# Kernel optimization log

Measured on AMD Instinct MI355X. Metric: run time of the kernel, lower is better.

The kernel has to match this reference:

```python
import jax, jax.numpy as jnp
import numpy as np

K_HOPS = 10
ALPHA = 0.1
N_NODES = 50000
N_EDGES = 600000
F_IN = 128
HIDDEN = 64
N_CLASSES = 40


def setup_inputs() -> dict:
    key = jax.random.key(0)
    k1, k2, k3, k4 = jax.random.split(key, 4)
    x = jax.random.normal(k1, (N_NODES, F_IN), dtype=jnp.float32)
    edge_index = jax.random.randint(k2, (2, N_EDGES), 0, N_NODES, dtype=jnp.int32)
    edge_weight = jnp.ones((N_EDGES,), dtype=jnp.float32)
    W1 = jax.random.normal(k3, (F_IN, HIDDEN), dtype=jnp.float32) * (1.0 / np.sqrt(F_IN))
    b1 = jnp.zeros((HIDDEN,), dtype=jnp.float32)
    W2 = jax.random.normal(k4, (HIDDEN, N_CLASSES), dtype=jnp.float32) * (1.0 / np.sqrt(HIDDEN))
    b2 = jnp.zeros((N_CLASSES,), dtype=jnp.float32)
    return {"x": x, "edge_index": edge_index, "edge_weight": edge_weight,
            "W1": W1, "b1": b1, "W2": W2, "b2": b2}


def reference(x, edge_index, edge_weight, W1, b1, W2, b2):
    n = x.shape[0]
    # GCN symmetric normalization with self-loops (tfg gcn cache)
    self_idx = jnp.arange(n, dtype=edge_index.dtype)
    row = jnp.concatenate([edge_index[0], self_idx])
    col = jnp.concatenate([edge_index[1], self_idx])
    w = jnp.concatenate([edge_weight, jnp.ones((n,), dtype=edge_weight.dtype)])
    deg = jax.ops.segment_sum(w, row, num_segments=n)
    dinv = jnp.where(deg > 0, jax.lax.rsqrt(jnp.maximum(deg, 1e-12)), 0.0)
    nw = dinv[row] * w * dinv[col]  # [E+N] normalized edge weights

    def prop(h):
        # h_out[i] = sum_{(i,j)} nw * h[j]
        return jax.ops.segment_sum(h[col] * nw[:, None], row, num_segments=n)

    def step(h, _):
        h_next = prop(h)
        return h_next, None

    # SSGC: out = (1-alpha)/K * sum_{l=1..K} T^l x + alpha * x
    def step_acc(carry, _):
        h, acc = carry
        h_next = prop(h)
        return (h_next, acc + h_next), None

    (_, acc), _ = jax.lax.scan(step_acc, (x, jnp.zeros_like(x)), None, length=K_HOPS)
    h = (1.0 - ALPHA) / K_HOPS * acc + ALPHA * x  # [N, F]

    h = jax.nn.relu(h @ W1 + b1)  # [N, HIDDEN]
    logits = h @ W2 + b2          # [N, N_CLASSES]
    return logits
```

## Files before the change

### kernel.cpp

```cpp
#include <hip/hip_runtime.h>
#include <hip/hip_fp16.h>
#include <math.h>

constexpr int   N   = 50000;
constexpr int   E   = 600000;
constexpr int   FIN = 128;
constexpr int   H   = 64;
constexpr int   C   = 40;
constexpr int   K   = 10;
constexpr float CK  = (1.0f - 0.1f) / 10.0f;
constexpr float AL  = 0.1f;

typedef float v2f __attribute__((ext_vector_type(2)));

__device__ __forceinline__ unsigned pack_fp8x4(float f0, float f1, float f2, float f3) {
    unsigned r = __builtin_amdgcn_cvt_pk_fp8_f32(f0, f1, 0u, false);
    r = __builtin_amdgcn_cvt_pk_fp8_f32(f2, f3, r, true);
    return r;
}

constexpr int G1N  = 64;
constexpr int XPAD = 132;
__global__ __launch_bounds__(256, 2) void k_gemm1(const float* __restrict__ x,
                                                  const float* __restrict__ W1,
                                                  float* __restrict__ y0,
                                                  unsigned char* __restrict__ y0f8) {
    __shared__ float ws[FIN * H];
    __shared__ float xs[G1N * XPAD];
    const float4* W14 = (const float4*)W1;
    const float4* x4  = (const float4*)x;
    int t = threadIdx.x;
    int node0 = blockIdx.x * G1N;
    for (int i = t; i < FIN * H / 4; i += 256) ((float4*)ws)[i] = W14[i];
    for (int p = 0; p < 8; ++p) {
        int idx = p * 256 + t;
        int n   = idx >> 5;
        int kk  = idx & 31;
        int node = node0 + n;
        float4 v = (node < N) ? x4[(size_t)node * (FIN / 4) + kk]
                              : make_float4(0.f, 0.f, 0.f, 0.f);
        *(float4*)(xs + n * XPAD + kk * 4) = v;
    }
    __syncthreads();
    int nb = (t >> 4) * 4;
    int cb = (t & 15) * 4;
    float a00=0,a01=0,a02=0,a03=0, a10=0,a11=0,a12=0,a13=0;
    float a20=0,a21=0,a22=0,a23=0, a30=0,a31=0,a32=0,a33=0;
#pragma unroll 8
    for (int k = 0; k < FIN; ++k) {
        float4 wv = *(const float4*)(ws + k * H + cb);
        float x0 = xs[(nb + 0) * XPAD + k];
        float x1 = xs[(nb + 1) * XPAD + k];
        float x2 = xs[(nb + 2) * XPAD + k];
        float x3 = xs[(nb + 3) * XPAD + k];
        a00 = fmaf(x0, wv.x, a00); a01 = fmaf(x0, wv.y, a01);
        a02 = fmaf(x0, wv.z, a02); a03 = fmaf(x0, wv.w, a03);
        a10 = fmaf(x1, wv.x, a10); a11 = fmaf(x1, wv.y, a11);
        a12 = fmaf(x1, wv.z, a12); a13 = fmaf(x1, wv.w, a13);
        a20 = fmaf(x2, wv.x, a20); a21 = fmaf(x2, wv.y, a21);
        a22 = fmaf(x2, wv.z, a22); a23 = fmaf(x2, wv.w, a23);
        a30 = fmaf(x3, wv.x, a30); a31 = fmaf(x3, wv.y, a31);
        a32 = fmaf(x3, wv.z, a32); a33 = fmaf(x3, wv.w, a33);
    }
    float4 rows[4] = {make_float4(a00,a01,a02,a03), make_float4(a10,a11,a12,a13),
                      make_float4(a20,a21,a22,a23), make_float4(a30,a31,a32,a33)};
#pragma unroll
    for (int i = 0; i < 4; ++i) {
        int node = node0 + nb + i;
        if (node >= N) break;
        float4 r = rows[i];
        *(float4*)(y0 + (size_t)node * H + cb) = r;
        *(unsigned*)(y0f8 + (size_t)node * H + cb) = pack_fp8x4(r.x, r.y, r.z, r.w);
    }
}

__global__ void k_count(const int* __restrict__ row, int* __restrict__ cnt8) {
    int e = blockIdx.x * blockDim.x + threadIdx.x;
    if (e >= E) return;
    atomicAdd(&cnt8[(size_t)(blockIdx.x & 7) * N + row[e]], 1);
}

__global__ __launch_bounds__(1024) void k_scan_blocks(const int* __restrict__ cnt8,
                                                      int* __restrict__ row_ptr,
                                                      int* __restrict__ bsum) {
    __shared__ int s[1024];
    int gid = blockIdx.x * 1024 + threadIdx.x;
    int v = 0;
    if (gid < N) {
#pragma unroll
        for (int c = 0; c < 8; ++c) v += cnt8[(size_t)c * N + gid];
    }
    s[threadIdx.x] = v;
    __syncthreads();
    for (int off = 1; off < 1024; off <<= 1) {
        int t = (threadIdx.x >= off) ? s[threadIdx.x - off] : 0;
        __syncthreads();
        s[threadIdx.x] += t;
        __syncthreads();
    }
    if (gid < N) row_ptr[gid] = s[threadIdx.x] - v;
    if (threadIdx.x == 1023) bsum[blockIdx.x] = s[1023];
}

__global__ void k_scan_sums(const int* __restrict__ bsum, int* __restrict__ boff, int nb) {
    int lane = threadIdx.x;
    int orig = (lane < nb) ? bsum[lane] : 0;
    int v = orig;
    for (int off = 1; off < 64; off <<= 1) {
        int t = __shfl_up(v, off, 64);
        if (lane >= off) v += t;
    }
    if (lane < nb) boff[lane] = v - orig;
}

__global__ __launch_bounds__(1024) void k_addoff(int* __restrict__ row_ptr,
                                                 const int* __restrict__ boff) {
    int gid = blockIdx.x * 1024 + threadIdx.x;
    if (gid < N) row_ptr[gid] += boff[blockIdx.x];
    if (gid == 0) row_ptr[N] = E;
}

__global__ void k_mkoff(const int* __restrict__ row_ptr, int* __restrict__ cnt8) {
    int i = blockIdx.x * blockDim.x + threadIdx.x;
    if (i >= N) return;
    int off = row_ptr[i];
#pragma unroll
    for (int c = 0; c < 8; ++c) {
        int t = cnt8[(size_t)c * N + i];
        cnt8[(size_t)c * N + i] = off;
        off += t;
    }
}

__global__ void k_scatter(const int* __restrict__ row, const int* __restrict__ col,
                          const float* __restrict__ w,
                          int* __restrict__ off8, int2* __restrict__ ep) {
    int e = blockIdx.x * blockDim.x + threadIdx.x;
    if (e >= E) return;
    int r = row[e];
    int p = atomicAdd(&off8[(size_t)(blockIdx.x & 7) * N + r], 1);
    ep[p] = make_int2(col[e], __float_as_int(w[e]));
}

__global__ void k_deg_dinv(const int2* __restrict__ ep, const int* __restrict__ row_ptr,
                           float* __restrict__ dinv, float* __restrict__ dinv2) {
    int i = blockIdx.x * blockDim.x + threadIdx.x;
    if (i >= N) return;
    float d = 1.0f;
    int e0 = row_ptr[i], e1 = row_ptr[i + 1];
    for (int j = e0; j < e1; ++j) d += __int_as_float(ep[j].y);
    float di = rsqrtf(d);
    dinv[i]  = di;
    dinv2[i] = di * di;
}

__global__ __launch_bounds__(256) void k_norm(int2* __restrict__ ep,
                                              const int* __restrict__ row_ptr,
                                              const float* __restrict__ dinv) {
    int node = blockIdx.x * 32 + (threadIdx.x >> 3);
    if (node >= N) return;
    int l = threadIdx.x & 7;
    float dr = dinv[node];
    int e0 = row_ptr[node], e1 = row_ptr[node + 1];
    for (int j = e0 + l; j < e1; j += 8) {
        int2 v = ep[j];
        ep[j] = make_int2(v.x, __float_as_int(__int_as_float(v.y) * dr * dinv[v.x]));
    }
}

constexpr int HSP = 68;
template <bool WRITE_H, bool ACC_INIT, bool FINAL>
__global__ __launch_bounds__(256) void k_prop(const uint2* __restrict__ hin,
                                              uint2* __restrict__ hout,
                                              __half* __restrict__ acch,
                                              const float* __restrict__ dinv2,
                                              const int* __restrict__ row_ptr,
                                              const int2* __restrict__ ep,
                                              const float4* __restrict__ y04,
                                              const float* __restrict__ b1,
                                              const float* __restrict__ W2,
                                              const float* __restrict__ b2,
                                              float* __restrict__ out) {
    extern __shared__ float smem[];
    float* w2s = smem;
    float* hs  = smem + H * C;
    float* b2s = hs + 32 * HSP;
    float* b1s = b2s + C;
    int t = threadIdx.x;
    if (FINAL) {
        for (int i = t; i < H * C; i += 256) w2s[i] = W2[i];
        if (t < C) b2s[t] = b2[t];
        if (t < H) b1s[t] = b1[t];
        __syncthreads();
    }
    int lane = t & 63;
    int nib  = (t >> 6) * 8 + (lane >> 3);
    int l    = lane & 7;
    int node = blockIdx.x * 32 + nib;
    bool nv  = node < N;
    int nodec = nv ? node : N - 1;
    int start = row_ptr[nodec];
    int deg   = nv ? (row_ptr[nodec + 1] - start) : 0;
    int md = deg;
    md = max(md, __shfl_xor(md, 8, 64));
    md = max(md, __shfl_xor(md, 16, 64));
    md = max(md, __shfl_xor(md, 32, 64));
    float s[8];
#pragma unroll
    for (int i = 0; i < 8; ++i) s[i] = 0.0f;
    auto accum = [&](uint2 v, float w) {
        v2f a0 = __builtin_amdgcn_cvt_pk_f32_fp8(v.x, false);
        v2f b0 = __builtin_amdgcn_cvt_pk_f32_fp8(v.x, true);
        v2f a1 = __builtin_amdgcn_cvt_pk_f32_fp8(v.y, false);
        v2f b1v = __builtin_amdgcn_cvt_pk_f32_fp8(v.y, true);
        s[0] = fmaf(w, a0.x, s[0]); s[1] = fmaf(w, a0.y, s[1]);
        s[2] = fmaf(w, b0.x, s[2]); s[3] = fmaf(w, b0.y, s[3]);
        s[4] = fmaf(w, a1.x, s[4]); s[5] = fmaf(w, a1.y, s[5]);
        s[6] = fmaf(w, b1v.x, s[6]); s[7] = fmaf(w, b1v.y, s[7]);
    };
    for (int j = 0; j < md; j += 2) {
        bool a0 = j < deg, a1 = j + 1 < deg;
        int2 e0 = ep[a0 ? start + j     : 0];
        int2 e1 = ep[a1 ? start + j + 1 : 0];
        uint2 v0 = hin[(size_t)e0.x * 8 + l];
        uint2 v1 = hin[(size_t)e1.x * 8 + l];
        float w0 = a0 ? __int_as_float(e0.y) : 0.0f;
        float w1 = a1 ? __int_as_float(e1.y) : 0.0f;
        accum(v0, w0);
        accum(v1, w1);
    }
    if (nv) {
        size_t base = (size_t)node * 8 + l;
        accum(hin[base], dinv2[node]);
        if (WRITE_H) {
            uint2 o;
            o.x = pack_fp8x4(s[0], s[1], s[2], s[3]);
            o.y = pack_fp8x4(s[4], s[5], s[6], s[7]);
            hout[base] = o;
        }
        uint4* ap = (uint4*)(acch + (size_t)node * H + l * 8);
        if (FINAL) {
            uint4 old = *ap;
            const unsigned* u = (const unsigned*)&old;
#pragma unroll
            for (int d = 0; d < 4; ++d) {
                float2 f = __half22float2(*(__half2*)&u[d]);
                s[2*d+0] += f.x; s[2*d+1] += f.y;
            }
            float4 ya = y04[(size_t)node * (H / 4) + 2 * l];
            float4 yb = y04[(size_t)node * (H / 4) + 2 * l + 1];
            const float* bp = b1s + l * 8;
            float* hp = hs + nib * HSP + l * 8;
            hp[0] = fmaxf(fmaf(CK, s[0], fmaf(AL, ya.x, bp[0])), 0.f);
            hp[1] = fmaxf(fmaf(CK, s[1], fmaf(AL, ya.y, bp[1])), 0.f);
            hp[2] = fmaxf(fmaf(CK, s[2], fmaf(AL, ya.z, bp[2])), 0.f);
            hp[3] = fmaxf(fmaf(CK, s[3], fmaf(AL, ya.w, bp[3])), 0.f);
            hp[4] = fmaxf(fmaf(CK, s[4], fmaf(AL, yb.x, bp[4])), 0.f);
            hp[5] = fmaxf(fmaf(CK, s[5], fmaf(AL, yb.y, bp[5])), 0.f);
            hp[6] = fmaxf(fmaf(CK, s[6], fmaf(AL, yb.z, bp[6])), 0.f);
            hp[7] = fmaxf(fmaf(CK, s[7], fmaf(AL, yb.w, bp[7])), 0.f);
        } else {
            if (!ACC_INIT) {
                uint4 old = *ap;
                const unsigned* u = (const unsigned*)&old;
#pragma unroll
                for (int d = 0; d < 4; ++d) {
                    float2 f = __half22float2(*(__half2*)&u[d]);
                    s[2*d+0] += f.x; s[2*d+1] += f.y;
                }
            }
            uint4 nvp;
            unsigned* u = (unsigned*)&nvp;
#pragma unroll
            for (int d = 0; d < 4; ++d) {
                __half2 h = __floats2half2_rn(s[2*d+0], s[2*d+1]);
                u[d] = *(unsigned*)&h;
            }
            *ap = nvp;
        }
    }
    if (FINAL) {
        __syncthreads();
        int node0 = blockIdx.x * 32;
        for (int o = t; o < 32 * C; o += 256) {
            int nl = o / C, c = o % C;
            int n2 = node0 + nl;
            if (n2 >= N) continue;
            float v = b2s[c];
            const float* hr = &hs[nl * HSP];
#pragma unroll
            for (int k = 0; k < H; ++k) v = fmaf(hr[k], w2s[k * C + c], v);
            out[n2 * C + c] = v;
        }
    }
}

extern "C" void kernel_launch(void* const* d_in, const int* in_sizes, int n_in,
                              void* d_out, int out_size, void* d_ws, size_t ws_size,
                              hipStream_t stream) {
    const float* x  = (const float*)d_in[0];
    const int*   ei = (const int*)d_in[1];
    const float* ew = (const float*)d_in[2];
    const float* W1 = (const float*)d_in[3];
    const float* b1 = (const float*)d_in[4];
    const float* W2 = (const float*)d_in[5];
    const float* b2 = (const float*)d_in[6];
    float* out = (float*)d_out;

    const int* row = ei;
    const int* col = ei + E;

    char* ws = (char*)d_ws;
    size_t off = 0;
    auto alloc = [&](size_t bytes) -> char* {
        char* p = ws + off;
        off = (off + bytes + 1023) & ~(size_t)1023;
        return p;
    };
    float*         y0   = (float*)alloc((size_t)N * H * 4);
    unsigned char* y0f8 = (unsigned char*)alloc((size_t)N * H);
    unsigned char* ha   = (unsigned char*)alloc((size_t)N * H);
    unsigned char* hb   = (unsigned char*)alloc((size_t)N * H);
    __half*        acch = (__half*)alloc((size_t)N * H * 2);
    int*   cnt8   = (int*)  alloc((size_t)8 * N * 4);
    float* dinv   = (float*)alloc((size_t)N * 4);
    float* dinv2  = (float*)alloc((size_t)N * 4);
    int*   row_ptr= (int*)  alloc((size_t)(N + 1) * 4);
    int*   bsum   = (int*)  alloc(64 * 4);
    int*   boff   = (int*)  alloc(64 * 4);
    int2*  ep     = (int2*) alloc((size_t)E * 8);

    hipMemsetAsync(cnt8, 0, (size_t)8 * N * 4, stream);

    k_gemm1<<<(N + G1N - 1) / G1N, 256, 0, stream>>>(x, W1, y0, y0f8);

    k_count<<<(E + 255) / 256, 256, 0, stream>>>(row, cnt8);

    constexpr int NB = (N + 1023) / 1024;
    k_scan_blocks<<<NB, 1024, 0, stream>>>(cnt8, row_ptr, bsum);
    k_scan_sums<<<1, 64, 0, stream>>>(bsum, boff, NB);
    k_addoff<<<NB, 1024, 0, stream>>>(row_ptr, boff);
    k_mkoff<<<(N + 255) / 256, 256, 0, stream>>>(row_ptr, cnt8);

    k_scatter<<<(E + 255) / 256, 256, 0, stream>>>(row, col, ew, cnt8, ep);
    k_deg_dinv<<<(N + 255) / 256, 256, 0, stream>>>(ep, row_ptr, dinv, dinv2);
    k_norm<<<(N + 31) / 32, 256, 0, stream>>>(ep, row_ptr, dinv);

    const uint2* hin = (const uint2*)y0f8;
    uint2* bufs[2] = {(uint2*)ha, (uint2*)hb};
    int grid = (N + 31) / 32;
    size_t smemF = (size_t)(H * C + 32 * HSP + C + H) * 4;
    for (int hop = 0; hop < K; ++hop) {
        uint2* hout = bufs[hop & 1];
        if (hop == 0)
            k_prop<true, true, false><<<grid, 256, 0, stream>>>(hin, hout, acch, dinv2,
                row_ptr, ep, (const float4*)y0, b1, W2, b2, out);
        else if (hop == K - 1)
            k_prop<false, false, true><<<grid, 256, smemF, stream>>>(hin, hout, acch, dinv2,
                row_ptr, ep, (const float4*)y0, b1, W2, b2, out);
        else
            k_prop<true, false, false><<<grid, 256, 0, stream>>>(hin, hout, acch, dinv2,
                row_ptr, ep, (const float4*)y0, b1, W2, b2, out);
        hin = hout;
    }
}
```

Measured before the change: 343.4 us.

## Fuse all propagation hops into persistent cooperative kernel with grid sync

Replaces the ten per-hop k_prop launches with a single cooperative kernel, k_hops. It keeps each node's running hop sum in registers across hops and uses grid.sync between hops. This removes the per-hop read and write of the fp16 accumulator buffer, as well as the launch gaps between hops. Each block owns 64 nodes and sorts them by degree so that the 8-lane node groups in a wavefront have similar trip counts. The trade-offs are the cost of nine grid-wide barriers and a requirement that all 782 blocks be co-resident. The occupancy check assumes 256 CUs; if it fails, the code falls back to the old multi-launch path.

```diff
diff --git a/kernel.cpp b/kernel.cpp
--- a/kernel.cpp
+++ b/kernel.cpp
@@ -1,6 +1,9 @@
 #include <hip/hip_runtime.h>
 #include <hip/hip_fp16.h>
+#include <hip/hip_cooperative_groups.h>
 #include <math.h>
+
+namespace cg = cooperative_groups;
 
 constexpr int   N   = 50000;
 constexpr int   E   = 600000;
@@ -168,7 +171,196 @@
     }
 }
 
-constexpr int HSP = 68;
+__device__ __forceinline__ void prop_chunk(const uint2* __restrict__ hin,
+                                           uint2* __restrict__ hout,
+                                           const int2* __restrict__ ep,
+                                           int start, int deg, int md,
+                                           float d2, int nc, bool nv, int l,
+                                           bool writeH, float* acc, float* sout) {
+    float s[8];
+#pragma unroll
+    for (int i = 0; i < 8; ++i) s[i] = 0.f;
+    for (int j = 0; j < md; j += 2) {
+        bool a0 = j < deg, a1 = j + 1 < deg;
+        int2 e0 = ep[a0 ? start + j     : 0];
+        int2 e1 = ep[a1 ? start + j + 1 : 0];
+        uint2 v0 = hin[(size_t)e0.x * 8 + l];
+        uint2 v1 = hin[(size_t)e1.x * 8 + l];
+        float w0 = a0 ? __int_as_float(e0.y) : 0.0f;
+        float w1 = a1 ? __int_as_float(e1.y) : 0.0f;
+        {
+            v2f p0 = __builtin_amdgcn_cvt_pk_f32_fp8(v0.x, false);
+            v2f p1 = __builtin_amdgcn_cvt_pk_f32_fp8(v0.x, true);
+            v2f p2 = __builtin_amdgcn_cvt_pk_f32_fp8(v0.y, false);
+            v2f p3 = __builtin_amdgcn_cvt_pk_f32_fp8(v0.y, true);
+            s[0] = fmaf(w0, p0.x, s[0]); s[1] = fmaf(w0, p0.y, s[1]);
+            s[2] = fmaf(w0, p1.x, s[2]); s[3] = fmaf(w0, p1.y, s[3]);
+            s[4] = fmaf(w0, p2.x, s[4]); s[5] = fmaf(w0, p2.y, s[5]);
+            s[6] = fmaf(w0, p3.x, s[6]); s[7] = fmaf(w0, p3.y, s[7]);
+        }
+        {
+            v2f p0 = __builtin_amdgcn_cvt_pk_f32_fp8(v1.x, false);
+            v2f p1 = __builtin_amdgcn_cvt_pk_f32_fp8(v1.x, true);
+            v2f p2 = __builtin_amdgcn_cvt_pk_f32_fp8(v1.y, false);
+            v2f p3 = __builtin_amdgcn_cvt_pk_f32_fp8(v1.y, true);
+            s[0] = fmaf(w1, p0.x, s[0]); s[1] = fmaf(w1, p0.y, s[1]);
+            s[2] = fmaf(w1, p1.x, s[2]); s[3] = fmaf(w1, p1.y, s[3]);
+            s[4] = fmaf(w1, p2.x, s[4]); s[5] = fmaf(w1, p2.y, s[5]);
+            s[6] = fmaf(w1, p3.x, s[6]); s[7] = fmaf(w1, p3.y, s[7]);
+        }
+    }
+    if (nv) {
+        uint2 hv = hin[(size_t)nc * 8 + l];
+        v2f p0 = __builtin_amdgcn_cvt_pk_f32_fp8(hv.x, false);
+        v2f p1 = __builtin_amdgcn_cvt_pk_f32_fp8(hv.x, true);
+        v2f p2 = __builtin_amdgcn_cvt_pk_f32_fp8(hv.y, false);
+        v2f p3 = __builtin_amdgcn_cvt_pk_f32_fp8(hv.y, true);
+        s[0] = fmaf(d2, p0.x, s[0]); s[1] = fmaf(d2, p0.y, s[1]);
+        s[2] = fmaf(d2, p1.x, s[2]); s[3] = fmaf(d2, p1.y, s[3]);
+        s[4] = fmaf(d2, p2.x, s[4]); s[5] = fmaf(d2, p2.y, s[5]);
+        s[6] = fmaf(d2, p3.x, s[6]); s[7] = fmaf(d2, p3.y, s[7]);
+        if (acc) {
+#pragma unroll
+            for (int i = 0; i < 8; ++i) acc[i] += s[i];
+        }
+        if (writeH) {
+            uint2 o;
+            o.x = pack_fp8x4(s[0], s[1], s[2], s[3]);
+            o.y = pack_fp8x4(s[4], s[5], s[6], s[7]);
+            hout[(size_t)nc * 8 + l] = o;
+        }
+    }
+    if (sout) {
+#pragma unroll
+        for (int i = 0; i < 8; ++i) sout[i] = s[i];
+    }
+}
+
+constexpr int NBLK = 782;
+constexpr int NPB  = 64;
+constexpr int HSP  = 68;
+
+__global__ __launch_bounds__(256, 4) void k_hops(const uint2* __restrict__ y0f8,
+                                                 uint2* __restrict__ ha,
+                                                 uint2* __restrict__ hb,
+                                                 const float* __restrict__ dinv2,
+                                                 const int* __restrict__ row_ptr,
+                                                 const int2* __restrict__ ep,
+                                                 const float4* __restrict__ y04,
+                                                 const float* __restrict__ b1,
+                                                 const float* __restrict__ W2,
+                                                 const float* __restrict__ b2,
+                                                 float* __restrict__ out) {
+    cg::grid_group grid = cg::this_grid();
+    __shared__ float w2s[H * C];
+    __shared__ float hs[NPB * HSP];
+    __shared__ float b2s[C];
+    __shared__ float b1s[H];
+    __shared__ int   s_deg[NPB];
+    __shared__ int   s_sorted[NPB];
+    int t = threadIdx.x;
+    int node0 = blockIdx.x * NPB;
+
+    for (int i = t; i < H * C; i += 256) w2s[i] = W2[i];
+    if (t < C) b2s[t] = b2[t];
+    if (t < H) b1s[t] = b1[t];
+
+    if (t < NPB) {
+        int n = node0 + t;
+        s_deg[t] = (n < N) ? row_ptr[n + 1] - row_ptr[n] : -1;
+    }
+    __syncthreads();
+    if (t < NPB) {
+        int d = s_deg[t];
+        int rank = 0;
+        for (int j = 0; j < NPB; ++j) {
+            int dj = s_deg[j];
+            rank += (dj < d) || (dj == d && j < t);
+        }
+        s_sorted[rank] = t;
+    }
+    __syncthreads();
+
+    int lane = t & 63;
+    int wv   = t >> 6;
+    int sub  = lane >> 3;
+    int l    = lane & 7;
+    int nibA = s_sorted[wv * 8 + sub];
+    int nibB = s_sorted[32 + wv * 8 + sub];
+    int nodeA = node0 + nibA;
+    int nodeB = node0 + nibB;
+    bool nvA = nodeA < N, nvB = nodeB < N;
+    int ncA = nvA ? nodeA : 0, ncB = nvB ? nodeB : 0;
+    int startA = row_ptr[ncA], degA = nvA ? (row_ptr[ncA + 1] - startA) : 0;
+    int startB = row_ptr[ncB], degB = nvB ? (row_ptr[ncB + 1] - startB) : 0;
+    float d2A = nvA ? dinv2[ncA] : 0.f;
+    float d2B = nvB ? dinv2[ncB] : 0.f;
+    int mdA = degA, mdB = degB;
+#pragma unroll
+    for (int off = 8; off <= 32; off <<= 1) {
+        mdA = max(mdA, __shfl_xor(mdA, off, 64));
+        mdB = max(mdB, __shfl_xor(mdB, off, 64));
+    }
+
+    float accA[8], accB[8];
+#pragma unroll
+    for (int i = 0; i < 8; ++i) { accA[i] = 0.f; accB[i] = 0.f; }
+
+    const uint2* hin = y0f8;
+    uint2* hbuf[2] = {ha, hb};
+
+    for (int hop = 0; hop < K; ++hop) {
+        uint2* hout = hbuf[hop & 1];
+        bool writeH = hop < K - 1;
+        prop_chunk(hin, hout, ep, startA, degA, mdA, d2A, ncA, nvA, l, writeH, accA, nullptr);
+        prop_chunk(hin, hout, ep, startB, degB, mdB, d2B, ncB, nvB, l, writeH, accB, nullptr);
+        if (hop < K - 1) {
+            grid.sync();
+            hin = hout;
+        }
+    }
+
+    if (nvA) {
+        float4 ya = y04[(size_t)ncA * (H / 4) + 2 * l];
+        float4 yb = y04[(size_t)ncA * (H / 4) + 2 * l + 1];
+        const float* bp = b1s + l * 8;
+        float* hp = hs + nibA * HSP + l * 8;
+        hp[0] = fmaxf(fmaf(CK, accA[0], fmaf(AL, ya.x, bp[0])), 0.f);
+        hp[1] = fmaxf(fmaf(CK, accA[1], fmaf(AL, ya.y, bp[1])), 0.f);
+        hp[2] = fmaxf(fmaf(CK, accA[2], fmaf(AL, ya.z, bp[2])), 0.f);
+        hp[3] = fmaxf(fmaf(CK, accA[3], fmaf(AL, ya.w, bp[3])), 0.f);
+        hp[4] = fmaxf(fmaf(CK, accA[4], fmaf(AL, yb.x, bp[4])), 0.f);
+        hp[5] = fmaxf(fmaf(CK, accA[5], fmaf(AL, yb.y, bp[5])), 0.f);
+        hp[6] = fmaxf(fmaf(CK, accA[6], fmaf(AL, yb.z, bp[6])), 0.f);
+        hp[7] = fmaxf(fmaf(CK, accA[7], fmaf(AL, yb.w, bp[7])), 0.f);
+    }
+    if (nvB) {
+        float4 ya = y04[(size_t)ncB * (H / 4) + 2 * l];
+        float4 yb = y04[(size_t)ncB * (H / 4) + 2 * l + 1];
+        const float* bp = b1s + l * 8;
+        float* hp = hs + nibB * HSP + l * 8;
+        hp[0] = fmaxf(fmaf(CK, accB[0], fmaf(AL, ya.x, bp[0])), 0.f);
+        hp[1] = fmaxf(fmaf(CK, accB[1], fmaf(AL, ya.y, bp[1])), 0.f);
+        hp[2] = fmaxf(fmaf(CK, accB[2], fmaf(AL, ya.z, bp[2])), 0.f);
+        hp[3] = fmaxf(fmaf(CK, accB[3], fmaf(AL, ya.w, bp[3])), 0.f);
+        hp[4] = fmaxf(fmaf(CK, accB[4], fmaf(AL, yb.x, bp[4])), 0.f);
+        hp[5] = fmaxf(fmaf(CK, accB[5], fmaf(AL, yb.y, bp[5])), 0.f);
+        hp[6] = fmaxf(fmaf(CK, accB[6], fmaf(AL, yb.z, bp[6])), 0.f);
+        hp[7] = fmaxf(fmaf(CK, accB[7], fmaf(AL, yb.w, bp[7])), 0.f);
+    }
+    __syncthreads();
+    for (int o = t; o < NPB * C; o += 256) {
+        int nl = o / C, c = o % C;
+        int n2 = node0 + nl;
+        if (n2 >= N) continue;
+        float v = b2s[c];
+        const float* hr = &hs[nl * HSP];
+#pragma unroll
+        for (int k = 0; k < H; ++k) v = fmaf(hr[k], w2s[k * C + c], v);
+        out[n2 * C + c] = v;
+    }
+}
+
 template <bool WRITE_H, bool ACC_INIT, bool FINAL>
 __global__ __launch_bounds__(256) void k_prop(const uint2* __restrict__ hin,
                                               uint2* __restrict__ hout,
@@ -202,43 +394,19 @@
     int start = row_ptr[nodec];
     int deg   = nv ? (row_ptr[nodec + 1] - start) : 0;
     int md = deg;
-    md = max(md, __shfl_xor(md, 8, 64));
-    md = max(md, __shfl_xor(md, 16, 64));
-    md = max(md, __shfl_xor(md, 32, 64));
+#pragma unroll
+    for (int off = 8; off <= 32; off <<= 1) md = max(md, __shfl_xor(md, off, 64));
     float s[8];
-#pragma unroll
-    for (int i = 0; i < 8; ++i) s[i] = 0.0f;
-    auto accum = [&](uint2 v, float w) {
-        v2f a0 = __builtin_amdgcn_cvt_pk_f32_fp8(v.x, false);
-        v2f b0 = __builtin_amdgcn_cvt_pk_f32_fp8(v.x, true);
-        v2f a1 = __builtin_amdgcn_cvt_pk_f32_fp8(v.y, false);
-        v2f b1v = __builtin_amdgcn_cvt_pk_f32_fp8(v.y, true);
-        s[0] = fmaf(w, a0.x, s[0]); s[1] = fmaf(w, a0.y, s[1]);
-        s[2] = fmaf(w, b0.x, s[2]); s[3] = fmaf(w, b0.y, s[3]);
-        s[4] = fmaf(w, a1.x, s[4]); s[5] = fmaf(w, a1.y, s[5]);
-        s[6] = fmaf(w, b1v.x, s[6]); s[7] = fmaf(w, b1v.y, s[7]);
-    };
-    for (int j = 0; j < md; j += 2) {
-        bool a0 = j < deg, a1 = j + 1 < deg;
-        int2 e0 = ep[a0 ? start + j     : 0];
-        int2 e1 = ep[a1 ? start + j + 1 : 0];
-        uint2 v0 = hin[(size_t)e0.x * 8 + l];
-        uint2 v1 = hin[(size_t)e1.x * 8 + l];
-        float w0 = a0 ? __int_as_float(e0.y) : 0.0f;
-        float w1 = a1 ? __int_as_float(e1.y) : 0.0f;
-        accum(v0, w0);
-        accum(v1, w1);
-    }
+    prop_chunk(hin, hout, ep, start, deg, md, nv ? dinv2[nodec] : 0.f, nodec, nv,
+               l, false, nullptr, s);
     if (nv) {
-        size_t base = (size_t)node * 8 + l;
-        accum(hin[base], dinv2[node]);
         if (WRITE_H) {
             uint2 o;
             o.x = pack_fp8x4(s[0], s[1], s[2], s[3]);
             o.y = pack_fp8x4(s[4], s[5], s[6], s[7]);
-            hout[base] = o;
-        }
-        uint4* ap = (uint4*)(acch + (size_t)node * H + l * 8);
+            hout[(size_t)nodec * 8 + l] = o;
+        }
+        uint4* ap = (uint4*)(acch + (size_t)nodec * H + l * 8);
         if (FINAL) {
             uint4 old = *ap;
             const unsigned* u = (const unsigned*)&old;
@@ -247,8 +415,8 @@
                 float2 f = __half22float2(*(__half2*)&u[d]);
                 s[2*d+0] += f.x; s[2*d+1] += f.y;
             }
-            float4 ya = y04[(size_t)node * (H / 4) + 2 * l];
-            float4 yb = y04[(size_t)node * (H / 4) + 2 * l + 1];
+            float4 ya = y04[(size_t)nodec * (H / 4) + 2 * l];
+            float4 yb = y04[(size_t)nodec * (H / 4) + 2 * l + 1];
             const float* bp = b1s + l * 8;
             float* hp = hs + nib * HSP + l * 8;
             hp[0] = fmaxf(fmaf(CK, s[0], fmaf(AL, ya.x, bp[0])), 0.f);
@@ -346,21 +514,39 @@
     k_deg_dinv<<<(N + 255) / 256, 256, 0, stream>>>(ep, row_ptr, dinv, dinv2);
     k_norm<<<(N + 31) / 32, 256, 0, stream>>>(ep, row_ptr, dinv);
 
-    const uint2* hin = (const uint2*)y0f8;
-    uint2* bufs[2] = {(uint2*)ha, (uint2*)hb};
-    int grid = (N + 31) / 32;
-    size_t smemF = (size_t)(H * C + 32 * HSP + C + H) * 4;
-    for (int hop = 0; hop < K; ++hop) {
-        uint2* hout = bufs[hop & 1];
-        if (hop == 0)
-            k_prop<true, true, false><<<grid, 256, 0, stream>>>(hin, hout, acch, dinv2,
-                row_ptr, ep, (const float4*)y0, b1, W2, b2, out);
-        else if (hop == K - 1)
-            k_prop<false, false, true><<<grid, 256, smemF, stream>>>(hin, hout, acch, dinv2,
-                row_ptr, ep, (const float4*)y0, b1, W2, b2, out);
-        else
-            k_prop<true, false, false><<<grid, 256, 0, stream>>>(hin, hout, acch, dinv2,
-                row_ptr, ep, (const float4*)y0, b1, W2, b2, out);
-        hin = hout;
-    }
-}
+    const uint2* y0f8c = (const uint2*)y0f8;
+    uint2* hac = (uint2*)ha;
+    uint2* hbc = (uint2*)hb;
+    const float4* y04 = (const float4*)y0;
+
+    int maxBlkPerCU = 0;
+    hipError_t oe = hipOccupancyMaxActiveBlocksPerMultiprocessor(&maxBlkPerCU,
+                                                                 k_hops, 256, 0);
+    bool coop_ok = (oe == hipSuccess) && ((long)maxBlkPerCU * 256 >= NBLK);
+
+    if (coop_ok) {
+        void* args[] = {(void*)&y0f8c, (void*)&hac, (void*)&hbc, (void*)&dinv2,
+                        (void*)&row_ptr, (void*)&ep, (void*)&y04, (void*)&b1,
+                        (void*)&W2, (void*)&b2, (void*)&out};
+        hipLaunchCooperativeKernel((const void*)k_hops, dim3(NBLK), dim3(256),
+                                   args, 0, stream);
+    } else {
+        const uint2* hin = y0f8c;
+        uint2* bufs[2] = {hac, hbc};
+        int grid = (N + 31) / 32;
+        size_t smemF = (size_t)(H * C + 32 * HSP + C + H) * 4;
+        for (int hop = 0; hop < K; ++hop) {
+            uint2* hout = bufs[hop & 1];
+            if (hop == 0)
+                k_prop<true, true, false><<<grid, 256, 0, stream>>>(hin, hout, acch, dinv2,
+                    row_ptr, ep, y04, b1, W2, b2, out);
+            else if (hop == K - 1)
+                k_prop<false, false, true><<<grid, 256, smemF, stream>>>(hin, hout, acch, dinv2,
+                    row_ptr, ep, y04, b1, W2, b2, out);
+            else
+                k_prop<true, false, false><<<grid, 256, 0, stream>>>(hin, hout, acch, dinv2,
+                    row_ptr, ep, y04, b1, W2, b2, out);
+            hin = hout;
+        }
+    }
+}
```

After: 342.9 us. Within noise of the previous version (-0.1%).
